# Optimization experiments

Measured on AMD Instinct MI355X. Metric: run time of the kernel, lower is better.

Reference implementation:

```python
import jax, jax.numpy as jnp
import numpy as np

M_FACTORS = [12, 8, 8]
N_FACTORS = [8, 8, 12]
E = 4          # hardcoded in original: gates.view(B, 4, 1, 1, 1)
R = 8          # TT rank
ALPHA = 16.0   # common_alpha
TAU = 1.0


def setup_inputs() -> dict:
    key = jax.random.key(0)
    ks = jax.random.split(key, 11)
    B, S, m = 32, 512, 768
    inp = {
        "X": jax.random.normal(ks[0], (B, S, m), jnp.float32),
        "router_w": jax.random.normal(ks[1], (E, m), jnp.float32) * 0.02,
        "router_b": jax.random.normal(ks[2], (E,), jnp.float32) * 0.02,
        "base_w": jax.random.normal(ks[3], (m, m), jnp.float32) * 0.02,
        "base_b": jax.random.normal(ks[4], (m,), jnp.float32) * 0.02,
        "core0": jax.random.normal(ks[5], (E, 1, 12, R), jnp.float32) * 0.1,
        "core1": jax.random.normal(ks[6], (E, R, 8, R), jnp.float32) * 0.1,
        "core2": jax.random.normal(ks[7], (E, R, 8, R), jnp.float32) * 0.1,
        "core3": jax.random.normal(ks[8], (E, R, 8, R), jnp.float32) * 0.1,
        "core4": jax.random.normal(ks[9], (E, R, 8, R), jnp.float32) * 0.1,
        "core5": jax.random.normal(ks[10], (E, R, 12, 1), jnp.float32) * 0.1,
    }
    return inp


def _gumbel_softmax_hard(logits, key):
    # torch.nn.functional.gumbel_softmax(logits, tau=TAU, hard=True)
    u = jax.random.uniform(key, logits.shape, logits.dtype, 1e-6, 1.0 - 1e-6)
    g = -jnp.log(-jnp.log(u))
    y_soft = jax.nn.softmax((logits + g) / TAU, axis=-1)
    y_hard = jax.nn.one_hot(jnp.argmax(y_soft, axis=-1), logits.shape[-1],
                            dtype=logits.dtype)
    # straight-through: y_hard - sg(y_soft) + y_soft
    return jax.lax.stop_gradient(y_hard - y_soft) + y_soft


def _tt_moe(X, gates, cores):
    # faithful to tensorized_multiplication_experts
    B, S, m = X.shape
    # [B, 1, S, m_factors[::-1]] -> last axis is m_factors[0]
    tt_state = X.reshape([B, 1, S] + M_FACTORS[::-1])
    num_m = len(M_FACTORS)
    for i in range(num_m):
        # per-sample expert-weighted core: [B, r, f, p]
        mc = jnp.einsum('be,erfp->brfp', gates, cores[i])
        tt_state = jnp.einsum('br...m,brmp->bp...', tt_state, mc)
    for i in range(len(N_FACTORS)):
        mc = jnp.einsum('be,erfp->brfp', gates, cores[num_m + i])
        tt_state = jnp.einsum('br...,brnp->bp...n', tt_state, mc)
    return tt_state.reshape(B, S, -1)  # trailing p == 1


def reference(X, router_w, router_b, base_w, base_b,
              core0, core1, core2, core3, core4, core5):
    cores = [core0, core1, core2, core3, core4, core5]
    pooled = X.mean(axis=1)                              # [B, m]
    logits = pooled @ router_w.T + router_b              # [B, E]
    gates = _gumbel_softmax_hard(logits, jax.random.key(42))
    base_out = X @ base_w.T + base_b                     # F.linear
    Z = _tt_moe(X, gates, cores)                         # [B, S, n]
    return Z * ALPHA + base_out
```

## Files before the change

### kernel.cpp

```cpp
#include <hip/hip_runtime.h>
#include <hip/hip_bf16.h>
#include <stdint.h>

#define GAS __attribute__((address_space(1)))
#define LAS __attribute__((address_space(3)))

typedef __attribute__((ext_vector_type(8))) short bf16x8;
typedef __attribute__((ext_vector_type(4))) float f32x4;

struct us4 { unsigned short x, y, z, w; };

__device__ __forceinline__ void gl_lds16(const void* g, void* lds) {
  __builtin_amdgcn_global_load_lds((const GAS unsigned int*)(uintptr_t)g,
                                   (LAS unsigned int*)(uintptr_t)lds, 16, 0, 0);
}

__device__ __forceinline__ unsigned short f2bf(float f) {
  unsigned u = __float_as_uint(f);
  return (unsigned short)((u + 0x7fffu + ((u >> 16) & 1u)) >> 16);
}

__device__ __forceinline__ void threefry2x32_42(unsigned x0, unsigned x1,
                                                unsigned* o0, unsigned* o1) {
  const unsigned k0 = 0u, k1 = 42u;
  unsigned ks[3] = {k0, k1, k0 ^ k1 ^ 0x1BD11BDAu};
  x0 += ks[0]; x1 += ks[1];
  const int rot[2][4] = {{13, 15, 26, 6}, {17, 29, 16, 24}};
#pragma unroll
  for (int i = 0; i < 5; ++i) {
#pragma unroll
    for (int j = 0; j < 4; ++j) {
      int r = rot[i & 1][j];
      x0 += x1;
      x1 = (x1 << r) | (x1 >> (32 - r));
      x1 ^= x0;
    }
    x0 += ks[(i + 1) % 3];
    x1 += ks[(i + 2) % 3] + (unsigned)(i + 1);
  }
  *o0 = x0; *o1 = x1;
}

__global__ __launch_bounds__(192) void k_router_pool(
    const float* __restrict__ X, const float* __restrict__ rw,
    unsigned short* __restrict__ Xbf, float* __restrict__ partial) {
  int t = threadIdx.x;
  int b = blockIdx.x >> 4, c = blockIdx.x & 15;
  int r0 = b * 512 + c * 32;
  const float* xp = X + (size_t)r0 * 768 + t * 4;
  unsigned short* xo = Xbf + (size_t)r0 * 768 + t * 4;
  float4 acc = {0.f, 0.f, 0.f, 0.f};
#pragma unroll 8
  for (int r = 0; r < 32; ++r) {
    float4 v = *reinterpret_cast<const float4*>(xp + (size_t)r * 768);
    acc.x += v.x; acc.y += v.y; acc.z += v.z; acc.w += v.w;
    us4 o;
    o.x = f2bf(v.x); o.y = f2bf(v.y); o.z = f2bf(v.z); o.w = f2bf(v.w);
    *reinterpret_cast<us4*>(xo + (size_t)r * 768) = o;
  }
  float lp[4];
#pragma unroll
  for (int e = 0; e < 4; ++e) {
    float4 w4 = *reinterpret_cast<const float4*>(rw + e * 768 + t * 4);
    lp[e] = acc.x * w4.x + acc.y * w4.y + acc.z * w4.z + acc.w * w4.w;
  }
#pragma unroll
  for (int off = 32; off > 0; off >>= 1) {
#pragma unroll
    for (int e = 0; e < 4; ++e) lp[e] += __shfl_down(lp[e], off);
  }
  __shared__ float red[3][4];
  int w = t >> 6;
  if ((t & 63) == 0) {
#pragma unroll
    for (int e = 0; e < 4; ++e) red[w][e] = lp[e];
  }
  __syncthreads();
  if (t < 4) partial[blockIdx.x * 4 + t] = red[0][t] + red[1][t] + red[2][t];
}

__global__ __launch_bounds__(256) void k_build(
    const float* __restrict__ c0, const float* __restrict__ c1,
    const float* __restrict__ c2, const float* __restrict__ c3,
    const float* __restrict__ c4, const float* __restrict__ c5,
    const float* __restrict__ bw, const float* __restrict__ partial,
    const float* __restrict__ rb, int* __restrict__ expert,
    unsigned short* __restrict__ Wbt) {
  int e = blockIdx.y, jc = blockIdx.x, t = threadIdx.x;

  if (jc == 0 && e == 0 && t < 128) {
    int b = t >> 2, ee = t & 3;
    float s = 0.f;
#pragma unroll
    for (int c = 0; c < 16; ++c) s += partial[(b * 16 + c) * 4 + ee];
    float lg = s * (1.0f / 512.0f) + rb[ee];
    int idx = b * 4 + ee;
    unsigned x0, x1;
    threefry2x32_42(0u, (unsigned)idx, &x0, &x1);
    unsigned bits = x0 ^ x1;
    float u01 = __uint_as_float((bits >> 9) | 0x3f800000u) - 1.0f;
    float u = u01 * ((1.0f - 1e-6f) - 1e-6f) + 1e-6f;
    u = fmaxf(u, 1e-6f);
    float v = lg + (-logf(-logf(u)));
    int bi = ee;
#pragma unroll
    for (int off = 1; off < 4; off <<= 1) {
      float vo = __shfl_xor(v, off);
      int io = __shfl_xor(bi, off);
      if (vo > v || (vo == v && io < bi)) { v = vo; bi = io; }
    }
    if (ee == 0) expert[b] = bi;
  }

  __shared__ float KA[768];
  __shared__ float LB[768];
  __shared__ float Kt[6144];
  __shared__ float LtS[128];

  for (int q = t; q < 768; q += 256) {
    int bc = q >> 3, p2 = q & 7;
    int b2 = bc / 12, cc = bc % 12;
    float s = 0.f;
#pragma unroll
    for (int p1 = 0; p1 < 8; ++p1)
      s += c0[e * 96 + cc * 8 + p1] * c1[((e * 8 + p1) * 8 + b2) * 8 + p2];
    KA[q] = s;
    int p4 = q / 96, mm = q % 96;
    int n2 = mm / 12, n3 = mm % 12;
    float s2 = 0.f;
#pragma unroll
    for (int p5 = 0; p5 < 8; ++p5)
      s2 += c4[((e * 8 + p4) * 8 + n2) * 8 + p5] * c5[(e * 8 + p5) * 12 + n3];
    LB[q] = s2;
  }
  __syncthreads();
  for (int q = t; q < 6144; q += 256) {
    int i = q >> 3, p3 = q & 7;
    int a = i / 96, bc = i % 96;
    float s = 0.f;
#pragma unroll
    for (int p2 = 0; p2 < 8; ++p2)
      s += KA[bc * 8 + p2] * c2[((e * 8 + p2) * 8 + a) * 8 + p3];
    Kt[p3 * 768 + i] = s;
  }
  if (t < 128) {
    int i = t >> 3, p3 = t & 7;
    int j = jc * 16 + i;
    int n1 = j / 96, mm = j % 96;
    float s2 = 0.f;
#pragma unroll
    for (int p4 = 0; p4 < 8; ++p4)
      s2 += c3[((e * 8 + p3) * 8 + n1) * 8 + p4] * LB[p4 * 96 + mm];
    LtS[i * 8 + p3] = s2;
  }
  __syncthreads();
  for (int idx = t; idx < 12288; idx += 256) {
    int jl = idx / 768, i = idx - jl * 768;
    int j = jc * 16 + jl;
    float s = 0.f;
#pragma unroll
    for (int p = 0; p < 8; ++p) s += Kt[p * 768 + i] * LtS[jl * 8 + p];
    float val = bw[(size_t)j * 768 + i] + 16.0f * s;
    Wbt[(size_t)e * 589824 + (size_t)j * 768 + i] = f2bf(val);
  }
}

__global__ __launch_bounds__(256) void k_gemm(
    const unsigned short* __restrict__ Xbf,
    const unsigned short* __restrict__ Wbt,
    const int* __restrict__ expert,
    const float* __restrict__ base_b,
    float* __restrict__ out)
{
  __shared__ unsigned short sA[2][8192];
  __shared__ unsigned short sB[2][8192];
  int tid = threadIdx.x;
  int w = tid >> 6, l = tid & 63;
  int l16 = l & 15, l4 = l >> 4;

  int bid = blockIdx.x;
  int work = (bid & 7) * 96 + (bid >> 3);
  int mtile = work / 6, ntile = work - mtile * 6;
  int m0 = mtile * 128, n0 = ntile * 128;
  int e = expert[mtile >> 2];
  const unsigned short* Wb = Wbt + (size_t)e * 589824;
  int wr = w >> 1, wc = w & 1;

  f32x4 acc[4][4];
#pragma unroll
  for (int i = 0; i < 4; ++i)
#pragma unroll
    for (int jj = 0; jj < 4; ++jj) acc[i][jj] = (f32x4)0.f;

  int rows[4], csw[4];
#pragma unroll
  for (int q = 0; q < 4; ++q) {
    int ci = (w * 4 + q) * 64 + l;
    rows[q] = ci >> 3;
    csw[q] = ((ci & 7) * 8) ^ ((rows[q] & 7) << 3);
  }

#define STAGE(bufi, k0)                                                        \
  {                                                                            \
    _Pragma("unroll") for (int q = 0; q < 4; ++q) {                            \
      const unsigned short* ga =                                               \
          Xbf + (size_t)(m0 + rows[q]) * 768 + (k0) + csw[q];                  \
      gl_lds16(ga, &sA[bufi][(w * 4 + q) * 512]);                              \
      const unsigned short* gb =                                               \
          Wb + (size_t)(n0 + rows[q]) * 768 + (k0) + csw[q];                   \
      gl_lds16(gb, &sB[bufi][(w * 4 + q) * 512]);                              \
    }                                                                          \
  }

  STAGE(0, 0);
  __syncthreads();

  int xorr = (l16 & 7) << 3;
  for (int kt = 0; kt < 12; ++kt) {
    int cur = kt & 1;
    if (kt < 11) STAGE(cur ^ 1, (kt + 1) * 64);
#pragma unroll
    for (int kk = 0; kk < 2; ++kk) {
      int coff = (kk * 32 + l4 * 8) ^ xorr;
      bf16x8 af[4], bfr[4];
#pragma unroll
      for (int am = 0; am < 4; ++am)
        af[am] = *reinterpret_cast<const bf16x8*>(
            &sA[cur][(wr * 64 + am * 16 + l16) * 64 + coff]);
#pragma unroll
      for (int bn = 0; bn < 4; ++bn)
        bfr[bn] = *reinterpret_cast<const bf16x8*>(
            &sB[cur][(wc * 64 + bn * 16 + l16) * 64 + coff]);
#pragma unroll
      for (int am = 0; am < 4; ++am)
#pragma unroll
        for (int bn = 0; bn < 4; ++bn)
          acc[am][bn] = __builtin_amdgcn_mfma_f32_16x16x32_bf16(bfr[bn], af[am], acc[am][bn], 0, 0, 0);
    }
    __syncthreads();
  }

  f32x4 bb4[4];
#pragma unroll
  for (int bn = 0; bn < 4; ++bn)
    bb4[bn] = *reinterpret_cast<const f32x4*>(base_b + n0 + wc * 64 + bn * 16 + l4 * 4);
#pragma unroll
  for (int am = 0; am < 4; ++am) {
    int m = m0 + wr * 64 + am * 16 + l16;
    float* op = out + (size_t)m * 768 + n0 + wc * 64 + l4 * 4;
#pragma unroll
    for (int bn = 0; bn < 4; ++bn) {
      f32x4 v = acc[am][bn] + bb4[bn];
      __builtin_nontemporal_store(v, reinterpret_cast<f32x4*>(op + bn * 16));
    }
  }
#undef STAGE
}

extern "C" void kernel_launch(void* const* d_in, const int* in_sizes, int n_in,
                              void* d_out, int out_size, void* d_ws, size_t ws_size,
                              hipStream_t stream) {
  const float* X  = (const float*)d_in[0];
  const float* rw = (const float*)d_in[1];
  const float* rb = (const float*)d_in[2];
  const float* bw = (const float*)d_in[3];
  const float* bb = (const float*)d_in[4];
  const float* c0 = (const float*)d_in[5];
  const float* c1 = (const float*)d_in[6];
  const float* c2 = (const float*)d_in[7];
  const float* c3 = (const float*)d_in[8];
  const float* c4 = (const float*)d_in[9];
  const float* c5 = (const float*)d_in[10];
  float* out = (float*)d_out;

  char* ws = (char*)d_ws;
  int* expert         = (int*)(ws + 0);
  float* partial      = (float*)(ws + 4096);
  unsigned short* Wbt = (unsigned short*)(ws + 262144);
  unsigned short* Xbf = (unsigned short*)(ws + 4980736);

  k_router_pool<<<512, 192, 0, stream>>>(X, rw, Xbf, partial);
  k_build<<<dim3(48, 4), 256, 0, stream>>>(c0, c1, c2, c3, c4, c5, bw,
                                           partial, rb, expert, Wbt);
  k_gemm<<<768, 256, 0, stream>>>(Xbf, Wbt, expert, bb, out);
}
```

Before: 64.84 us.

## Merge pooling and weight-build kernels, compute gating inside GEMM, single-buffer LDS

Fuses the router pooling/bf16 conversion kernel and the per-expert weight build kernel into one launch, with block ranges picking the role, so the two independent jobs run concurrently. The gumbel argmax expert selection moves into each GEMM block, which removes the third launch dependency and the expert buffer. The GEMM drops LDS double buffering and requests 4 blocks per CU. That gives up load/compute overlap inside a block in exchange for more blocks in flight and fewer launches.

Result: faster. 58.85 us (-9.2%).

```diff
diff --git a/kernel.cpp b/kernel.cpp
--- a/kernel.cpp
+++ b/kernel.cpp
@@ -41,60 +41,140 @@
   *o0 = x0; *o1 = x1;
 }
 
-__global__ __launch_bounds__(192) void k_router_pool(
+__global__ __launch_bounds__(256) void k_prep(
     const float* __restrict__ X, const float* __restrict__ rw,
-    unsigned short* __restrict__ Xbf, float* __restrict__ partial) {
-  int t = threadIdx.x;
-  int b = blockIdx.x >> 4, c = blockIdx.x & 15;
-  int r0 = b * 512 + c * 32;
-  const float* xp = X + (size_t)r0 * 768 + t * 4;
-  unsigned short* xo = Xbf + (size_t)r0 * 768 + t * 4;
-  float4 acc = {0.f, 0.f, 0.f, 0.f};
-#pragma unroll 8
-  for (int r = 0; r < 32; ++r) {
-    float4 v = *reinterpret_cast<const float4*>(xp + (size_t)r * 768);
-    acc.x += v.x; acc.y += v.y; acc.z += v.z; acc.w += v.w;
-    us4 o;
-    o.x = f2bf(v.x); o.y = f2bf(v.y); o.z = f2bf(v.z); o.w = f2bf(v.w);
-    *reinterpret_cast<us4*>(xo + (size_t)r * 768) = o;
-  }
-  float lp[4];
-#pragma unroll
-  for (int e = 0; e < 4; ++e) {
-    float4 w4 = *reinterpret_cast<const float4*>(rw + e * 768 + t * 4);
-    lp[e] = acc.x * w4.x + acc.y * w4.y + acc.z * w4.z + acc.w * w4.w;
-  }
-#pragma unroll
-  for (int off = 32; off > 0; off >>= 1) {
-#pragma unroll
-    for (int e = 0; e < 4; ++e) lp[e] += __shfl_down(lp[e], off);
-  }
-  __shared__ float red[3][4];
-  int w = t >> 6;
-  if ((t & 63) == 0) {
-#pragma unroll
-    for (int e = 0; e < 4; ++e) red[w][e] = lp[e];
-  }
-  __syncthreads();
-  if (t < 4) partial[blockIdx.x * 4 + t] = red[0][t] + red[1][t] + red[2][t];
-}
-
-__global__ __launch_bounds__(256) void k_build(
+    const float* __restrict__ bw,
     const float* __restrict__ c0, const float* __restrict__ c1,
     const float* __restrict__ c2, const float* __restrict__ c3,
     const float* __restrict__ c4, const float* __restrict__ c5,
-    const float* __restrict__ bw, const float* __restrict__ partial,
-    const float* __restrict__ rb, int* __restrict__ expert,
+    unsigned short* __restrict__ Xbf, float* __restrict__ partial,
     unsigned short* __restrict__ Wbt) {
-  int e = blockIdx.y, jc = blockIdx.x, t = threadIdx.x;
-
-  if (jc == 0 && e == 0 && t < 128) {
-    int b = t >> 2, ee = t & 3;
+  __shared__ __align__(16) char smem[31232];
+  int t = threadIdx.x;
+  int bid = blockIdx.x;
+
+  if (bid < 192) {
+    int e = bid / 48, jc = bid % 48;
+    float* KA = (float*)smem;
+    float* LB = (float*)(smem + 3072);
+    float* Kt = (float*)(smem + 6144);
+    float* LtS = (float*)(smem + 30720);
+    for (int q = t; q < 768; q += 256) {
+      int bc = q >> 3, p2 = q & 7;
+      int b2 = bc / 12, cc = bc % 12;
+      float s = 0.f;
+#pragma unroll
+      for (int p1 = 0; p1 < 8; ++p1)
+        s += c0[e * 96 + cc * 8 + p1] * c1[((e * 8 + p1) * 8 + b2) * 8 + p2];
+      KA[q] = s;
+      int p4 = q / 96, mm = q % 96;
+      int n2 = mm / 12, n3 = mm % 12;
+      float s2 = 0.f;
+#pragma unroll
+      for (int p5 = 0; p5 < 8; ++p5)
+        s2 += c4[((e * 8 + p4) * 8 + n2) * 8 + p5] * c5[(e * 8 + p5) * 12 + n3];
+      LB[q] = s2;
+    }
+    __syncthreads();
+    for (int q = t; q < 6144; q += 256) {
+      int i = q >> 3, p3 = q & 7;
+      int a = i / 96, bc = i % 96;
+      float s = 0.f;
+#pragma unroll
+      for (int p2 = 0; p2 < 8; ++p2)
+        s += KA[bc * 8 + p2] * c2[((e * 8 + p2) * 8 + a) * 8 + p3];
+      Kt[p3 * 768 + i] = s;
+    }
+    if (t < 128) {
+      int i = t >> 3, p3 = t & 7;
+      int j = jc * 16 + i;
+      int n1 = j / 96, mm = j % 96;
+      float s2 = 0.f;
+#pragma unroll
+      for (int p4 = 0; p4 < 8; ++p4)
+        s2 += c3[((e * 8 + p3) * 8 + n1) * 8 + p4] * LB[p4 * 96 + mm];
+      LtS[i * 8 + p3] = s2;
+    }
+    __syncthreads();
+    for (int idx = t; idx < 12288; idx += 256) {
+      int jl = idx / 768, i = idx - jl * 768;
+      int j = jc * 16 + jl;
+      float s = 0.f;
+#pragma unroll
+      for (int p = 0; p < 8; ++p) s += Kt[p * 768 + i] * LtS[jl * 8 + p];
+      float val = bw[(size_t)j * 768 + i] + 16.0f * s;
+      Wbt[(size_t)e * 589824 + (size_t)j * 768 + i] = f2bf(val);
+    }
+  } else {
+    float* red = (float*)smem;
+    int p = bid - 192;
+    int r0 = p * 32;
+    float lp0 = 0.f, lp1 = 0.f, lp2 = 0.f, lp3 = 0.f;
+    if (t < 192) {
+      const float* xp = X + (size_t)r0 * 768 + t * 4;
+      unsigned short* xo = Xbf + (size_t)r0 * 768 + t * 4;
+      float4 acc = {0.f, 0.f, 0.f, 0.f};
+#pragma unroll 8
+      for (int r = 0; r < 32; ++r) {
+        float4 v = *reinterpret_cast<const float4*>(xp + (size_t)r * 768);
+        acc.x += v.x; acc.y += v.y; acc.z += v.z; acc.w += v.w;
+        us4 o;
+        o.x = f2bf(v.x); o.y = f2bf(v.y); o.z = f2bf(v.z); o.w = f2bf(v.w);
+        *reinterpret_cast<us4*>(xo + (size_t)r * 768) = o;
+      }
+      float4 w0 = *reinterpret_cast<const float4*>(rw + 0 * 768 + t * 4);
+      float4 w1 = *reinterpret_cast<const float4*>(rw + 1 * 768 + t * 4);
+      float4 w2 = *reinterpret_cast<const float4*>(rw + 2 * 768 + t * 4);
+      float4 w3 = *reinterpret_cast<const float4*>(rw + 3 * 768 + t * 4);
+      lp0 = acc.x * w0.x + acc.y * w0.y + acc.z * w0.z + acc.w * w0.w;
+      lp1 = acc.x * w1.x + acc.y * w1.y + acc.z * w1.z + acc.w * w1.w;
+      lp2 = acc.x * w2.x + acc.y * w2.y + acc.z * w2.z + acc.w * w2.w;
+      lp3 = acc.x * w3.x + acc.y * w3.y + acc.z * w3.z + acc.w * w3.w;
+    }
+#pragma unroll
+    for (int off = 32; off > 0; off >>= 1) {
+      lp0 += __shfl_down(lp0, off);
+      lp1 += __shfl_down(lp1, off);
+      lp2 += __shfl_down(lp2, off);
+      lp3 += __shfl_down(lp3, off);
+    }
+    int w = t >> 6;
+    if ((t & 63) == 0 && w < 3) {
+      red[w * 4 + 0] = lp0; red[w * 4 + 1] = lp1;
+      red[w * 4 + 2] = lp2; red[w * 4 + 3] = lp3;
+    }
+    __syncthreads();
+    if (t < 4) partial[p * 4 + t] = red[0 + t] + red[4 + t] + red[8 + t];
+  }
+}
+
+__global__ __launch_bounds__(256, 4) void k_gemm(
+    const unsigned short* __restrict__ Xbf,
+    const unsigned short* __restrict__ Wbt,
+    const float* __restrict__ partial,
+    const float* __restrict__ rb,
+    const float* __restrict__ base_b,
+    float* __restrict__ out)
+{
+  __shared__ unsigned short sA[128 * 64];
+  __shared__ unsigned short sB[128 * 64];
+  __shared__ int sExp;
+  int t = threadIdx.x;
+  int w = t >> 6, l = t & 63;
+  int l16 = l & 15, l4 = l >> 4;
+
+  int bid = blockIdx.x;
+  int work = (bid & 7) * 96 + (bid >> 3);
+  int mtile = work / 6, ntile = work - mtile * 6;
+  int m0 = mtile * 128, n0 = ntile * 128;
+  int b = mtile >> 2;
+
+  if (t < 4) {
     float s = 0.f;
 #pragma unroll
-    for (int c = 0; c < 16; ++c) s += partial[(b * 16 + c) * 4 + ee];
-    float lg = s * (1.0f / 512.0f) + rb[ee];
-    int idx = b * 4 + ee;
+    for (int c = 0; c < 16; ++c) s += partial[(b * 16 + c) * 4 + t];
+    float lg = s * (1.0f / 512.0f) + rb[t];
+    int idx = b * 4 + t;
     unsigned x0, x1;
     threefry2x32_42(0u, (unsigned)idx, &x0, &x1);
     unsigned bits = x0 ^ x1;
@@ -102,87 +182,17 @@
     float u = u01 * ((1.0f - 1e-6f) - 1e-6f) + 1e-6f;
     u = fmaxf(u, 1e-6f);
     float v = lg + (-logf(-logf(u)));
-    int bi = ee;
+    int bi = t;
 #pragma unroll
     for (int off = 1; off < 4; off <<= 1) {
       float vo = __shfl_xor(v, off);
       int io = __shfl_xor(bi, off);
       if (vo > v || (vo == v && io < bi)) { v = vo; bi = io; }
     }
-    if (ee == 0) expert[b] = bi;
-  }
-
-  __shared__ float KA[768];
-  __shared__ float LB[768];
-  __shared__ float Kt[6144];
-  __shared__ float LtS[128];
-
-  for (int q = t; q < 768; q += 256) {
-    int bc = q >> 3, p2 = q & 7;
-    int b2 = bc / 12, cc = bc % 12;
-    float s = 0.f;
-#pragma unroll
-    for (int p1 = 0; p1 < 8; ++p1)
-      s += c0[e * 96 + cc * 8 + p1] * c1[((e * 8 + p1) * 8 + b2) * 8 + p2];
-    KA[q] = s;
-    int p4 = q / 96, mm = q % 96;
-    int n2 = mm / 12, n3 = mm % 12;
-    float s2 = 0.f;
-#pragma unroll
-    for (int p5 = 0; p5 < 8; ++p5)
-      s2 += c4[((e * 8 + p4) * 8 + n2) * 8 + p5] * c5[(e * 8 + p5) * 12 + n3];
-    LB[q] = s2;
+    if (t == 0) sExp = bi;
   }
   __syncthreads();
-  for (int q = t; q < 6144; q += 256) {
-    int i = q >> 3, p3 = q & 7;
-    int a = i / 96, bc = i % 96;
-    float s = 0.f;
-#pragma unroll
-    for (int p2 = 0; p2 < 8; ++p2)
-      s += KA[bc * 8 + p2] * c2[((e * 8 + p2) * 8 + a) * 8 + p3];
-    Kt[p3 * 768 + i] = s;
-  }
-  if (t < 128) {
-    int i = t >> 3, p3 = t & 7;
-    int j = jc * 16 + i;
-    int n1 = j / 96, mm = j % 96;
-    float s2 = 0.f;
-#pragma unroll
-    for (int p4 = 0; p4 < 8; ++p4)
-      s2 += c3[((e * 8 + p3) * 8 + n1) * 8 + p4] * LB[p4 * 96 + mm];
-    LtS[i * 8 + p3] = s2;
-  }
-  __syncthreads();
-  for (int idx = t; idx < 12288; idx += 256) {
-    int jl = idx / 768, i = idx - jl * 768;
-    int j = jc * 16 + jl;
-    float s = 0.f;
-#pragma unroll
-    for (int p = 0; p < 8; ++p) s += Kt[p * 768 + i] * LtS[jl * 8 + p];
-    float val = bw[(size_t)j * 768 + i] + 16.0f * s;
-    Wbt[(size_t)e * 589824 + (size_t)j * 768 + i] = f2bf(val);
-  }
-}
-
-__global__ __launch_bounds__(256) void k_gemm(
-    const unsigned short* __restrict__ Xbf,
-    const unsigned short* __restrict__ Wbt,
-    const int* __restrict__ expert,
-    const float* __restrict__ base_b,
-    float* __restrict__ out)
-{
-  __shared__ unsigned short sA[2][8192];
-  __shared__ unsigned short sB[2][8192];
-  int tid = threadIdx.x;
-  int w = tid >> 6, l = tid & 63;
-  int l16 = l & 15, l4 = l >> 4;
-
-  int bid = blockIdx.x;
-  int work = (bid & 7) * 96 + (bid >> 3);
-  int mtile = work / 6, ntile = work - mtile * 6;
-  int m0 = mtile * 128, n0 = ntile * 128;
-  int e = expert[mtile >> 2];
+  int e = sExp;
   const unsigned short* Wb = Wbt + (size_t)e * 589824;
   int wr = w >> 1, wc = w & 1;
 
@@ -200,25 +210,16 @@
     csw[q] = ((ci & 7) * 8) ^ ((rows[q] & 7) << 3);
   }
 
-#define STAGE(bufi, k0)                                                        \
-  {                                                                            \
-    _Pragma("unroll") for (int q = 0; q < 4; ++q) {                            \
-      const unsigned short* ga =                                               \
-          Xbf + (size_t)(m0 + rows[q]) * 768 + (k0) + csw[q];                  \
-      gl_lds16(ga, &sA[bufi][(w * 4 + q) * 512]);                              \
-      const unsigned short* gb =                                               \
-          Wb + (size_t)(n0 + rows[q]) * 768 + (k0) + csw[q];                   \
-      gl_lds16(gb, &sB[bufi][(w * 4 + q) * 512]);                              \
-    }                                                                          \
-  }
-
-  STAGE(0, 0);
-  __syncthreads();
-
   int xorr = (l16 & 7) << 3;
-  for (int kt = 0; kt < 12; ++kt) {
-    int cur = kt & 1;
-    if (kt < 11) STAGE(cur ^ 1, (kt + 1) * 64);
+  for (int k0 = 0; k0 < 768; k0 += 64) {
+#pragma unroll
+    for (int q = 0; q < 4; ++q) {
+      const unsigned short* ga = Xbf + (size_t)(m0 + rows[q]) * 768 + k0 + csw[q];
+      gl_lds16(ga, &sA[(w * 4 + q) * 512]);
+      const unsigned short* gb = Wb + (size_t)(n0 + rows[q]) * 768 + k0 + csw[q];
+      gl_lds16(gb, &sB[(w * 4 + q) * 512]);
+    }
+    __syncthreads();
 #pragma unroll
     for (int kk = 0; kk < 2; ++kk) {
       int coff = (kk * 32 + l4 * 8) ^ xorr;
@@ -226,16 +227,17 @@
 #pragma unroll
       for (int am = 0; am < 4; ++am)
         af[am] = *reinterpret_cast<const bf16x8*>(
-            &sA[cur][(wr * 64 + am * 16 + l16) * 64 + coff]);
+            &sA[(wr * 64 + am * 16 + l16) * 64 + coff]);
 #pragma unroll
       for (int bn = 0; bn < 4; ++bn)
         bfr[bn] = *reinterpret_cast<const bf16x8*>(
-            &sB[cur][(wc * 64 + bn * 16 + l16) * 64 + coff]);
+            &sB[(wc * 64 + bn * 16 + l16) * 64 + coff]);
 #pragma unroll
       for (int am = 0; am < 4; ++am)
 #pragma unroll
         for (int bn = 0; bn < 4; ++bn)
-          acc[am][bn] = __builtin_amdgcn_mfma_f32_16x16x32_bf16(bfr[bn], af[am], acc[am][bn], 0, 0, 0);
+          acc[am][bn] = __builtin_amdgcn_mfma_f32_16x16x32_bf16(
+              bfr[bn], af[am], acc[am][bn], 0, 0, 0);
     }
     __syncthreads();
   }
@@ -254,7 +256,6 @@
       __builtin_nontemporal_store(v, reinterpret_cast<f32x4*>(op + bn * 16));
     }
   }
-#undef STAGE
 }
 
 extern "C" void kernel_launch(void* const* d_in, const int* in_sizes, int n_in,
@@ -274,13 +275,11 @@
   float* out = (float*)d_out;
 
   char* ws = (char*)d_ws;
-  int* expert         = (int*)(ws + 0);
   float* partial      = (float*)(ws + 4096);
   unsigned short* Wbt = (unsigned short*)(ws + 262144);
   unsigned short* Xbf = (unsigned short*)(ws + 4980736);
 
-  k_router_pool<<<512, 192, 0, stream>>>(X, rw, Xbf, partial);
-  k_build<<<dim3(48, 4), 256, 0, stream>>>(c0, c1, c2, c3, c4, c5, bw,
-                                           partial, rb, expert, Wbt);
-  k_gemm<<<768, 256, 0, stream>>>(Xbf, Wbt, expert, bb, out);
-}
+  k_prep<<<704, 256, 0, stream>>>(X, rw, bw, c0, c1, c2, c3, c4, c5,
+                                  Xbf, partial, Wbt);
+  k_gemm<<<768, 256, 0, stream>>>(Xbf, Wbt, partial, rb, bb, out);
+}
```
